# Kernel optimization log

Measured on AMD Instinct MI355X. Metric: run time of the kernel, lower is better.

## Reference

```python
import jax, jax.numpy as jnp
import numpy as np

D_MODEL = 1024
NUM_HEADS = 16
HEAD_DIM = D_MODEL // NUM_HEADS


def setup_inputs() -> dict:
    key = jax.random.key(0)
    ks = jax.random.split(key, 10)
    s = 1.0 / np.sqrt(D_MODEL)
    return {
        "x": jax.random.normal(ks[0], (2, 2048, D_MODEL), dtype=jnp.float32),
        "Wq": jax.random.normal(ks[1], (D_MODEL, D_MODEL), dtype=jnp.float32) * s,
        "bq": jnp.zeros((D_MODEL,), jnp.float32),
        "Wk": jax.random.normal(ks[2], (D_MODEL, D_MODEL), dtype=jnp.float32) * s,
        "bk": jnp.zeros((D_MODEL,), jnp.float32),
        "Wv": jax.random.normal(ks[3], (D_MODEL, D_MODEL), dtype=jnp.float32) * s,
        "bv": jnp.zeros((D_MODEL,), jnp.float32),
        "Wo": jax.random.normal(ks[4], (D_MODEL, D_MODEL), dtype=jnp.float32) * s,
        "bo": jnp.zeros((D_MODEL,), jnp.float32),
        "rotary": jax.random.normal(ks[5], (1, 1, HEAD_DIM), dtype=jnp.float32) * 0.02,
    }


def reference(x, Wq, bq, Wk, bk, Wv, bv, Wo, bo, rotary):
    B, S, _ = x.shape
    H, Dh = NUM_HEADS, HEAD_DIM
    q = (x @ Wq + bq).reshape(B, S, H, Dh)
    k = (x @ Wk + bk).reshape(B, S, H, Dh)
    v = (x @ Wv + bv).reshape(B, S, H, Dh)
    # additive learned bias broadcast over (B, S, H) -> rotary has shape (1,1,Dh)
    q_rot = q + rotary[:, :, None, :]  # (B,S,H,Dh)
    scale = 1.0 / jnp.sqrt(jnp.asarray(Dh, jnp.float32))
    attn = jnp.einsum('bqhd,bkhd->bhqk', q_rot, k) * scale
    attn = jax.nn.softmax(attn, axis=-1)  # dropout is identity in eval / p=0
    out = jnp.einsum('bhqk,bkhd->bqhd', attn, v).reshape(B, S, H * Dh)
    return out @ Wo + bo
```

## Files before the change

### kernel.cpp

```cpp
#include <hip/hip_runtime.h>
#include <hip/hip_bf16.h>
#include <hip/hip_fp16.h>
#include <cstdint>

typedef _Float16 f16;
typedef _Float16 f16x4 __attribute__((ext_vector_type(4)));
typedef _Float16 f16x8 __attribute__((ext_vector_type(8)));
typedef __fp16 h16x2 __attribute__((ext_vector_type(2)));
typedef float f32x4 __attribute__((ext_vector_type(4)));

constexpr int D_MODEL = 1024;
constexpr int NH = 16;
constexpr int DH = 64;
constexpr int BATCH = 2;
constexpr int SEQ = 2048;
constexpr int NTOK = BATCH * SEQ;

static __device__ __forceinline__ void gld_lds16(const void* g, void* l) {
  __builtin_amdgcn_global_load_lds(
      (__attribute__((address_space(1))) void*)(g),
      (__attribute__((address_space(3))) void*)(l), 16, 0, 0);
}

static __device__ __forceinline__ f16x4 pack4(float a, float b, float c, float d) {
  h16x2 lo = __builtin_amdgcn_cvt_pkrtz(a, b);
  h16x2 hi = __builtin_amdgcn_cvt_pkrtz(c, d);
  struct { h16x2 x, y; } pr{lo, hi};
  return __builtin_bit_cast(f16x4, pr);
}


__global__ void cvt_x(const float* __restrict__ x, f16* __restrict__ xh) {
  int i = blockIdx.x * blockDim.x + threadIdx.x;
  const float4* p = reinterpret_cast<const float4*>(x) + (size_t)i * 2;
  float4 a = p[0], b = p[1];
  f16x8 o;
  o[0] = (f16)a.x; o[1] = (f16)a.y; o[2] = (f16)a.z; o[3] = (f16)a.w;
  o[4] = (f16)b.x; o[5] = (f16)b.y; o[6] = (f16)b.z; o[7] = (f16)b.w;
  *reinterpret_cast<f16x8*>(xh + (size_t)i * 8) = o;
}

__global__ void cvt_w(const float* __restrict__ Wq, const float* __restrict__ Wk,
                      const float* __restrict__ Wv, const float* __restrict__ Wo,
                      f16* __restrict__ Wqkvt, f16* __restrict__ Wot) {
  __shared__ float tile[32][33];
  int z = blockIdx.z;
  const float* src = (z == 0) ? Wq : (z == 1) ? Wk : (z == 2) ? Wv : Wo;
  f16* dst = (z < 3) ? (Wqkvt + (size_t)z * D_MODEL * D_MODEL) : Wot;
  int n0 = blockIdx.x * 32, k0 = blockIdx.y * 32;
  int tx = threadIdx.x & 31, ty = threadIdx.x >> 5;
#pragma unroll
  for (int j = 0; j < 32; j += 8)
    tile[ty + j][tx] = src[(size_t)(k0 + ty + j) * D_MODEL + n0 + tx];
  __syncthreads();
#pragma unroll
  for (int j = 0; j < 32; j += 8)
    dst[(size_t)(n0 + ty + j) * D_MODEL + k0 + tx] = (f16)tile[tx][ty + j];
}

__global__ void transpose_v(const f16* __restrict__ V, f16* __restrict__ Vt) {
  __shared__ __align__(16) f16 t[64 * 64];
  const int bh = blockIdx.y, s0 = blockIdx.x * 64;
  const f16* src = V + ((size_t)bh * SEQ + s0) * DH;
  f16* dst = Vt + (size_t)bh * DH * SEQ + s0;
  const int i = threadIdx.x;
#pragma unroll
  for (int p = 0; p < 2; ++p) {
    int seg = p * 256 + i;
    int s = seg >> 3, d0 = (seg & 7) * 8;
    f16x8 v = *reinterpret_cast<const f16x8*>(src + (size_t)s * DH + d0);
#pragma unroll
    for (int j = 0; j < 8; ++j) {
      int d = d0 + j;
      int swz = ((s >> 3) ^ (d & 7) ^ ((d >> 3) & 7)) & 7;
      t[d * 64 + swz * 8 + (s & 7)] = v[j];
    }
  }
  __syncthreads();
#pragma unroll
  for (int p = 0; p < 2; ++p) {
    int seg = p * 256 + i;
    int d = seg >> 3, c0 = (seg & 7) * 8;
    int swz = ((c0 >> 3) ^ (d & 7) ^ ((d >> 3) & 7)) & 7;
    f16x8 v = *reinterpret_cast<const f16x8*>(&t[d * 64 + swz * 8]);
    *reinterpret_cast<f16x8*>(dst + (size_t)d * SEQ + c0) = v;
  }
}


template <int MODE, int BM>
__global__ __launch_bounds__(256, 3) void gemm128(
    const f16* __restrict__ A, const f16* __restrict__ Bt,
    const float* __restrict__ b0, const float* __restrict__ rot,
    f16* __restrict__ oq, f16* __restrict__ ok, f16* __restrict__ ov,
    float* __restrict__ oOut) {
  constexpr int K = 1024;
  constexpr int BK = 64;
  constexpr int MI = BM / 32;
  constexpr int NBY = 4096 / BM;
  constexpr int CBY = NBY / 8;
  __shared__ __align__(16) f16 As[BM * BK];
  __shared__ __align__(16) f16 Bs[128 * BK];
  const int tid = threadIdx.x;
  const int w = tid >> 6, lane = tid & 63;
  const int flat = blockIdx.x;
  const int xcd = flat & 7, i0 = flat >> 3;
  const int by = xcd * CBY + (i0 % CBY);
  const int bx = i0 / CBY;
  const int m0 = by * BM, n0 = bx * 128;
  const int wr = (w >> 1) * (BM / 2), wc = (w & 1) * 64;
  const int lr = lane & 15, lg = lane >> 4;

  f32x4 acc[MI][4] = {};

  auto stage = [&](int kt) {
#pragma unroll
    for (int i = 0; i < MI; ++i) {
      int seg = (w * MI + i) * 64 + lane;
      int row = seg >> 3, c = seg & 7;
      int col = (c ^ (row & 7)) * 8;
      gld_lds16(A + (size_t)(m0 + row) * K + kt + col, &As[seg * 8]);
    }
#pragma unroll
    for (int i = 0; i < 4; ++i) {
      int seg = (w * 4 + i) * 64 + lane;
      int row = seg >> 3, c = seg & 7;
      int col = (c ^ (row & 7)) * 8;
      gld_lds16(Bt + (size_t)(n0 + row) * K + kt + col, &Bs[seg * 8]);
    }
  };

  stage(0);
#pragma unroll 1
  for (int kt = 0; kt < K; kt += BK) {
    __syncthreads();
#pragma unroll
    for (int kk2 = 0; kk2 < 2; ++kk2) {
      f16x8 af[MI], bf[4];
#pragma unroll
      for (int mi = 0; mi < MI; ++mi)
        af[mi] = *reinterpret_cast<const f16x8*>(
            &As[(wr + mi * 16 + lr) * BK + ((kk2 * 4 + lg) ^ (lr & 7)) * 8]);
#pragma unroll
      for (int ni = 0; ni < 4; ++ni)
        bf[ni] = *reinterpret_cast<const f16x8*>(
            &Bs[(wc + ni * 16 + lr) * BK + ((kk2 * 4 + lg) ^ (lr & 7)) * 8]);
#pragma unroll
      for (int mi = 0; mi < MI; ++mi)
#pragma unroll
        for (int ni = 0; ni < 4; ++ni)
          acc[mi][ni] = __builtin_amdgcn_mfma_f32_16x16x32_f16(af[mi], bf[ni], acc[mi][ni], 0, 0, 0);
    }
    __syncthreads();
    if (kt + BK < K) stage(kt + BK);
  }

#pragma unroll
  for (int mi = 0; mi < MI; ++mi) {
    int rowb = m0 + wr + mi * 16 + lg * 4;
#pragma unroll
    for (int ni = 0; ni < 4; ++ni) {
      int col = n0 + wc + ni * 16 + lr;
#pragma unroll
      for (int r = 0; r < 4; ++r) {
        float val = acc[mi][ni][r];
        int m = rowb + r;
        if (MODE == 0) {
          int which = col >> 10, rest = col & 1023;
          int hh = rest >> 6, d = rest & 63;
          int bb = m >> 11, ss = m & 2047;
          size_t dst = ((size_t)(bb * NH + hh) * SEQ + ss) * DH + d;
          if (which == 0) {
            oq[dst] = (f16)((val + b0[rest] + rot[d]) * (0.125f * 1.4426950408889634f));
          } else if (which == 1) {
            ok[dst] = (f16)(val + b0[1024 + rest]);
          } else {
            ov[dst] = (f16)(val + b0[2048 + rest]);
          }
        } else {
          oOut[(size_t)m * D_MODEL + col] = val + b0[col];
        }
      }
    }
  }
}

__global__ void cat_bias(const float* __restrict__ bq, const float* __restrict__ bk,
                         const float* __restrict__ bv, float* __restrict__ bqkv) {
  int i = blockIdx.x * blockDim.x + threadIdx.x;
  bqkv[i] = bq[i];
  bqkv[1024 + i] = bk[i];
  bqkv[2048 + i] = bv[i];
}

__global__ __launch_bounds__(256, 2) void attn(
    const f16* __restrict__ Qg, const f16* __restrict__ Kg,
    const f16* __restrict__ Vtg, f16* __restrict__ Og) {
  __shared__ __align__(16) f16 Ks[2][64 * 64];
  __shared__ __align__(16) f16 Vs[2][64 * 64];
  __shared__ __align__(16) f16 Ps[4][32 * 64];
  const int tid = threadIdx.x, w = tid >> 6, lane = tid & 63;
  const int lr = lane & 15, lg = lane >> 4;
  const int b = blockIdx.x;
  const int xcd = b & 7, j = b >> 3;
  const int bh = xcd * 4 + (j & 3);
  const int qb = j >> 2;
  const int q0 = qb * 128 + w * 32;
  const f16* Qb = Qg + (size_t)bh * SEQ * DH;
  const f16* Kb = Kg + (size_t)bh * SEQ * DH;
  const f16* Vtb = Vtg + (size_t)bh * DH * SEQ;

  f16x8 aq[2][2];
#pragma unroll
  for (int qf = 0; qf < 2; ++qf)
#pragma unroll
    for (int ks = 0; ks < 2; ++ks)
      aq[qf][ks] = *reinterpret_cast<const f16x8*>(
          Qb + (size_t)(q0 + qf * 16 + lr) * DH + ks * 32 + lg * 8);

  float mi[2] = {-1e30f, -1e30f}, li[2] = {0.f, 0.f};
  f32x4 accO[2][4] = {};

  auto stage = [&](int buf, int t) {
#pragma unroll
    for (int i = 0; i < 2; ++i) {
      int seg = (w * 2 + i) * 64 + lane;
      int row = seg >> 3, c = seg & 7;
      int sc8 = (c ^ (row & 7)) * 8;
      gld_lds16(Kb + (size_t)(t + row) * DH + sc8, &Ks[buf][seg * 8]);
      gld_lds16(Vtb + (size_t)row * SEQ + t + sc8, &Vs[buf][seg * 8]);
    }
  };

  stage(0, 0);
  int cur = 0;
#pragma unroll 1
  for (int t = 0; t < SEQ; t += 64) {
    __syncthreads();
    if (t + 64 < SEQ) stage(cur ^ 1, t + 64);

    f32x4 sc[2][4];
#pragma unroll
    for (int kt2 = 0; kt2 < 4; ++kt2) {
      f32x4 z0 = {}, z1 = {};
#pragma unroll
      for (int ks = 0; ks < 2; ++ks) {
        f16x8 kf = *reinterpret_cast<const f16x8*>(
            &Ks[cur][(kt2 * 16 + lr) * 64 + ((ks * 4 + lg) ^ (lr & 7)) * 8]);
        z0 = __builtin_amdgcn_mfma_f32_16x16x32_f16(kf, aq[0][ks], z0, 0, 0, 0);
        z1 = __builtin_amdgcn_mfma_f32_16x16x32_f16(kf, aq[1][ks], z1, 0, 0, 0);
      }
      sc[0][kt2] = z0;
      sc[1][kt2] = z1;
    }

#pragma unroll
    for (int qf = 0; qf < 2; ++qf) {
      float pm = sc[qf][0][0];
#pragma unroll
      for (int kt2 = 0; kt2 < 4; ++kt2)
#pragma unroll
        for (int r = 0; r < 4; ++r) pm = fmaxf(pm, sc[qf][kt2][r]);
      pm = fmaxf(pm, __shfl_xor(pm, 16));
      pm = fmaxf(pm, __shfl_xor(pm, 32));
      if (!__all(pm <= mi[qf] + 8.f)) {
        float nm = fmaxf(mi[qf], pm);
        float s8 = __builtin_amdgcn_exp2f(mi[qf] - nm);
        mi[qf] = nm;
        li[qf] *= s8;
#pragma unroll
        for (int ct = 0; ct < 4; ++ct)
#pragma unroll
          for (int r = 0; r < 4; ++r) accO[qf][ct][r] *= s8;
      }
      float rs = 0.f;
#pragma unroll
      for (int kt2 = 0; kt2 < 4; ++kt2)
#pragma unroll
        for (int r = 0; r < 4; ++r) {
          float p = __builtin_amdgcn_exp2f(sc[qf][kt2][r] - mi[qf]);
          sc[qf][kt2][r] = p;
          rs += p;
        }
      rs += __shfl_xor(rs, 16);
      rs += __shfl_xor(rs, 32);
      li[qf] += rs;
#pragma unroll
      for (int kt2 = 0; kt2 < 4; ++kt2) {
        f16x4 pk = pack4(sc[qf][kt2][0], sc[qf][kt2][1], sc[qf][kt2][2], sc[qf][kt2][3]);
        int addr = (qf * 16 + lr) * 64 +
                   (((kt2 * 2 + (lg >> 1)) ^ (lr & 7)) * 8) + (lg & 1) * 4;
        *reinterpret_cast<f16x4*>(&Ps[w][addr]) = pk;
      }
    }

#pragma unroll
    for (int ks = 0; ks < 2; ++ks) {
      f16x8 ap0 = *reinterpret_cast<const f16x8*>(
          &Ps[w][lr * 64 + ((ks * 4 + lg) ^ (lr & 7)) * 8]);
      f16x8 ap1 = *reinterpret_cast<const f16x8*>(
          &Ps[w][(16 + lr) * 64 + ((ks * 4 + lg) ^ (lr & 7)) * 8]);
#pragma unroll
      for (int ct = 0; ct < 4; ++ct) {
        f16x8 bv = *reinterpret_cast<const f16x8*>(
            &Vs[cur][(ct * 16 + lr) * 64 + ((ks * 4 + lg) ^ (lr & 7)) * 8]);
        accO[0][ct] = __builtin_amdgcn_mfma_f32_16x16x32_f16(bv, ap0, accO[0][ct], 0, 0, 0);
        accO[1][ct] = __builtin_amdgcn_mfma_f32_16x16x32_f16(bv, ap1, accO[1][ct], 0, 0, 0);
      }
    }
    cur ^= 1;
  }

  const int bb = bh >> 4, hh = bh & 15;
#pragma unroll
  for (int qf = 0; qf < 2; ++qf) {
    float inv = 1.f / li[qf];
    f16* dst = Og + (size_t)(bb * SEQ + q0 + qf * 16 + lr) * D_MODEL + hh * DH;
#pragma unroll
    for (int ct = 0; ct < 4; ++ct) {
      f16x4 pk = pack4(accO[qf][ct][0] * inv, accO[qf][ct][1] * inv,
                       accO[qf][ct][2] * inv, accO[qf][ct][3] * inv);
      *reinterpret_cast<f16x4*>(dst + ct * 16 + lg * 4) = pk;
    }
  }
}


extern "C" void kernel_launch(void* const* d_in, const int* in_sizes, int n_in,
                              void* d_out, int out_size, void* d_ws, size_t ws_size,
                              hipStream_t stream) {
  const float* x  = (const float*)d_in[0];
  const float* Wq = (const float*)d_in[1];
  const float* bq = (const float*)d_in[2];
  const float* Wk = (const float*)d_in[3];
  const float* bk = (const float*)d_in[4];
  const float* Wv = (const float*)d_in[5];
  const float* bv = (const float*)d_in[6];
  const float* Wo = (const float*)d_in[7];
  const float* bo = (const float*)d_in[8];
  const float* rot = (const float*)d_in[9];

  char* wsb = (char*)d_ws;
  f16* Xh    = (f16*)(wsb);
  f16* Wqkvt = (f16*)(wsb + ((size_t)8 << 20));
  f16* Wot   = (f16*)(wsb + ((size_t)14 << 20));
  f16* Qa    = (f16*)(wsb + ((size_t)16 << 20));
  f16* Ka    = (f16*)(wsb + ((size_t)24 << 20));
  f16* Va    = (f16*)(wsb + ((size_t)32 << 20));
  f16* Oa    = (f16*)(wsb + ((size_t)40 << 20));
  f16* Vta   = (f16*)(wsb + ((size_t)48 << 20));
  float* bqkv = (float*)(wsb + ((size_t)56 << 20));

  cvt_x<<<dim3(NTOK * D_MODEL / (8 * 256)), dim3(256), 0, stream>>>(x, Xh);
  cvt_w<<<dim3(32, 32, 4), dim3(256), 0, stream>>>(Wq, Wk, Wv, Wo, Wqkvt, Wot);
  cat_bias<<<dim3(4), dim3(256), 0, stream>>>(bq, bk, bv, bqkv);

  gemm128<0, 128><<<dim3(768), dim3(256), 0, stream>>>(
      Xh, Wqkvt, bqkv, rot, Qa, Ka, Va, nullptr);

  transpose_v<<<dim3(SEQ / 64, BATCH * NH), dim3(256), 0, stream>>>(Va, Vta);

  attn<<<dim3((SEQ / 128) * BATCH * NH), dim3(256), 0, stream>>>(Qa, Ka, Vta, Oa);

  gemm128<1, 64><<<dim3(512), dim3(256), 0, stream>>>(
      Oa, Wot, bo, nullptr, nullptr, nullptr, nullptr, (float*)d_out);
}
```

Before: 216.8 us.

## Drop LDS staging in attention, load K/V fragments directly; write V transposed in GEMM

The QKV GEMM epilogue now writes V straight into the transposed [bh][d][s] layout, so the separate transpose_v kernel is removed. The attention kernel stops staging K and V tiles through LDS with barriers. Each wave instead loads its MFMA fragments from global memory into registers, with K double-buffered in registers one tile ahead. The block-to-(head, query-block) mapping is also changed so blocks of the same head sit on one XCD. This removes a kernel launch and the LDS sync traffic, but each of the four waves now reloads the same K/V from global/L2, and the V transposed stores from the GEMM are strided.

Result: slower. 275.8 us (+27.2%).

```diff
diff --git a/kernel.cpp b/kernel.cpp
--- a/kernel.cpp
+++ b/kernel.cpp
@@ -56,35 +56,6 @@
 #pragma unroll
   for (int j = 0; j < 32; j += 8)
     dst[(size_t)(n0 + ty + j) * D_MODEL + k0 + tx] = (f16)tile[tx][ty + j];
-}
-
-__global__ void transpose_v(const f16* __restrict__ V, f16* __restrict__ Vt) {
-  __shared__ __align__(16) f16 t[64 * 64];
-  const int bh = blockIdx.y, s0 = blockIdx.x * 64;
-  const f16* src = V + ((size_t)bh * SEQ + s0) * DH;
-  f16* dst = Vt + (size_t)bh * DH * SEQ + s0;
-  const int i = threadIdx.x;
-#pragma unroll
-  for (int p = 0; p < 2; ++p) {
-    int seg = p * 256 + i;
-    int s = seg >> 3, d0 = (seg & 7) * 8;
-    f16x8 v = *reinterpret_cast<const f16x8*>(src + (size_t)s * DH + d0);
-#pragma unroll
-    for (int j = 0; j < 8; ++j) {
-      int d = d0 + j;
-      int swz = ((s >> 3) ^ (d & 7) ^ ((d >> 3) & 7)) & 7;
-      t[d * 64 + swz * 8 + (s & 7)] = v[j];
-    }
-  }
-  __syncthreads();
-#pragma unroll
-  for (int p = 0; p < 2; ++p) {
-    int seg = p * 256 + i;
-    int d = seg >> 3, c0 = (seg & 7) * 8;
-    int swz = ((c0 >> 3) ^ (d & 7) ^ ((d >> 3) & 7)) & 7;
-    f16x8 v = *reinterpret_cast<const f16x8*>(&t[d * 64 + swz * 8]);
-    *reinterpret_cast<f16x8*>(dst + (size_t)d * SEQ + c0) = v;
-  }
 }
 
 
@@ -169,13 +140,13 @@
           int which = col >> 10, rest = col & 1023;
           int hh = rest >> 6, d = rest & 63;
           int bb = m >> 11, ss = m & 2047;
-          size_t dst = ((size_t)(bb * NH + hh) * SEQ + ss) * DH + d;
           if (which == 0) {
-            oq[dst] = (f16)((val + b0[rest] + rot[d]) * (0.125f * 1.4426950408889634f));
+            oq[((size_t)(bb * NH + hh) * SEQ + ss) * DH + d] =
+                (f16)((val + b0[rest] + rot[d]) * (0.125f * 1.4426950408889634f));
           } else if (which == 1) {
-            ok[dst] = (f16)(val + b0[1024 + rest]);
+            ok[((size_t)(bb * NH + hh) * SEQ + ss) * DH + d] = (f16)(val + b0[1024 + rest]);
           } else {
-            ov[dst] = (f16)(val + b0[2048 + rest]);
+            ov[((size_t)(bb * NH + hh) * DH + d) * SEQ + ss] = (f16)(val + b0[2048 + rest]);
           }
         } else {
           oOut[(size_t)m * D_MODEL + col] = val + b0[col];
@@ -196,15 +167,13 @@
 __global__ __launch_bounds__(256, 2) void attn(
     const f16* __restrict__ Qg, const f16* __restrict__ Kg,
     const f16* __restrict__ Vtg, f16* __restrict__ Og) {
-  __shared__ __align__(16) f16 Ks[2][64 * 64];
-  __shared__ __align__(16) f16 Vs[2][64 * 64];
   __shared__ __align__(16) f16 Ps[4][32 * 64];
   const int tid = threadIdx.x, w = tid >> 6, lane = tid & 63;
   const int lr = lane & 15, lg = lane >> 4;
   const int b = blockIdx.x;
   const int xcd = b & 7, j = b >> 3;
-  const int bh = xcd * 4 + (j & 3);
-  const int qb = j >> 2;
+  const int bh = xcd * 4 + (j >> 4);
+  const int qb = j & 15;
   const int q0 = qb * 128 + w * 32;
   const f16* Qb = Qg + (size_t)bh * SEQ * DH;
   const f16* Kb = Kg + (size_t)bh * SEQ * DH;
@@ -220,24 +189,24 @@
 
   float mi[2] = {-1e30f, -1e30f}, li[2] = {0.f, 0.f};
   f32x4 accO[2][4] = {};
-
-  auto stage = [&](int buf, int t) {
-#pragma unroll
-    for (int i = 0; i < 2; ++i) {
-      int seg = (w * 2 + i) * 64 + lane;
-      int row = seg >> 3, c = seg & 7;
-      int sc8 = (c ^ (row & 7)) * 8;
-      gld_lds16(Kb + (size_t)(t + row) * DH + sc8, &Ks[buf][seg * 8]);
-      gld_lds16(Vtb + (size_t)row * SEQ + t + sc8, &Vs[buf][seg * 8]);
+  f16x8 kfA[8], kfB[8], bv[8];
+
+  auto loadK = [&](f16x8* kf, int t) {
+#pragma unroll
+    for (int i = 0; i < 8; ++i) {
+      int kt2 = i >> 1, ks = i & 1;
+      kf[i] = *reinterpret_cast<const f16x8*>(
+          Kb + (size_t)(t + kt2 * 16 + lr) * DH + ks * 32 + lg * 8);
     }
   };
 
-  stage(0, 0);
-  int cur = 0;
-#pragma unroll 1
-  for (int t = 0; t < SEQ; t += 64) {
-    __syncthreads();
-    if (t + 64 < SEQ) stage(cur ^ 1, t + 64);
+  auto doTile = [&](f16x8* kf, f16x8* kfn, int t) {
+#pragma unroll
+    for (int i = 0; i < 8; ++i) {
+      int ct = i >> 1, ks = i & 1;
+      bv[i] = *reinterpret_cast<const f16x8*>(
+          Vtb + (size_t)(ct * 16 + lr) * SEQ + t + ks * 32 + lg * 8);
+    }
 
     f32x4 sc[2][4];
 #pragma unroll
@@ -245,14 +214,14 @@
       f32x4 z0 = {}, z1 = {};
 #pragma unroll
       for (int ks = 0; ks < 2; ++ks) {
-        f16x8 kf = *reinterpret_cast<const f16x8*>(
-            &Ks[cur][(kt2 * 16 + lr) * 64 + ((ks * 4 + lg) ^ (lr & 7)) * 8]);
-        z0 = __builtin_amdgcn_mfma_f32_16x16x32_f16(kf, aq[0][ks], z0, 0, 0, 0);
-        z1 = __builtin_amdgcn_mfma_f32_16x16x32_f16(kf, aq[1][ks], z1, 0, 0, 0);
+        z0 = __builtin_amdgcn_mfma_f32_16x16x32_f16(kf[kt2 * 2 + ks], aq[0][ks], z0, 0, 0, 0);
+        z1 = __builtin_amdgcn_mfma_f32_16x16x32_f16(kf[kt2 * 2 + ks], aq[1][ks], z1, 0, 0, 0);
       }
       sc[0][kt2] = z0;
       sc[1][kt2] = z1;
     }
+
+    if (t + 64 < SEQ) loadK(kfn, t + 64);
 
 #pragma unroll
     for (int qf = 0; qf < 2; ++qf) {
@@ -302,13 +271,17 @@
           &Ps[w][(16 + lr) * 64 + ((ks * 4 + lg) ^ (lr & 7)) * 8]);
 #pragma unroll
       for (int ct = 0; ct < 4; ++ct) {
-        f16x8 bv = *reinterpret_cast<const f16x8*>(
-            &Vs[cur][(ct * 16 + lr) * 64 + ((ks * 4 + lg) ^ (lr & 7)) * 8]);
-        accO[0][ct] = __builtin_amdgcn_mfma_f32_16x16x32_f16(bv, ap0, accO[0][ct], 0, 0, 0);
-        accO[1][ct] = __builtin_amdgcn_mfma_f32_16x16x32_f16(bv, ap1, accO[1][ct], 0, 0, 0);
-      }
-    }
-    cur ^= 1;
+        accO[0][ct] = __builtin_amdgcn_mfma_f32_16x16x32_f16(bv[ct * 2 + ks], ap0, accO[0][ct], 0, 0, 0);
+        accO[1][ct] = __builtin_amdgcn_mfma_f32_16x16x32_f16(bv[ct * 2 + ks], ap1, accO[1][ct], 0, 0, 0);
+      }
+    }
+  };
+
+  loadK(kfA, 0);
+#pragma unroll 1
+  for (int t = 0; t < SEQ; t += 128) {
+    doTile(kfA, kfB, t);
+    doTile(kfB, kfA, t + 64);
   }
 
   const int bb = bh >> 4, hh = bh & 15;
@@ -346,7 +319,6 @@
   f16* Wot   = (f16*)(wsb + ((size_t)14 << 20));
   f16* Qa    = (f16*)(wsb + ((size_t)16 << 20));
   f16* Ka    = (f16*)(wsb + ((size_t)24 << 20));
-  f16* Va    = (f16*)(wsb + ((size_t)32 << 20));
   f16* Oa    = (f16*)(wsb + ((size_t)40 << 20));
   f16* Vta   = (f16*)(wsb + ((size_t)48 << 20));
   float* bqkv = (float*)(wsb + ((size_t)56 << 20));
@@ -356,9 +328,7 @@
   cat_bias<<<dim3(4), dim3(256), 0, stream>>>(bq, bk, bv, bqkv);
 
   gemm128<0, 128><<<dim3(768), dim3(256), 0, stream>>>(
-      Xh, Wqkvt, bqkv, rot, Qa, Ka, Va, nullptr);
-
-  transpose_v<<<dim3(SEQ / 64, BATCH * NH), dim3(256), 0, stream>>>(Va, Vta);
+      Xh, Wqkvt, bqkv, rot, Qa, Ka, Vta, nullptr);
 
   attn<<<dim3((SEQ / 128) * BATCH * NH), dim3(256), 0, stream>>>(Qa, Ka, Vta, Oa);
 
```
